# Kernel optimization log

Hardware: AMD Instinct MI355X
Metric: run time of the kernel (lower is better)

Reference implementation:

```python
import jax, jax.numpy as jnp
import numpy as np

CAPACITY_FACTOR = 1.0


def setup_inputs() -> dict:
    key = jax.random.key(0)
    k1, k2, k3 = jax.random.split(key, 3)
    x = jax.random.normal(k1, (4, 2048, 2048), jnp.float32)          # [B, S, d_model]
    wg = jax.random.normal(k2, (2048, 8), jnp.float32) * 0.02        # gate weight [d_model, E]
    we = jax.random.normal(k3, (8, 2048, 8192), jnp.float32) * 0.02  # expert weights [E, d_model, d_ff]
    be = jnp.zeros((8, 8192), jnp.float32)                           # expert bias [E, d_ff]
    return {"x": x, "wg": wg, "we": we, "be": be}


def reference(x, wg, we, be):
    d = x.shape[-1]
    tokens = x.reshape(-1, d)                       # [S, d]  (S = total tokens)
    S = tokens.shape[0]
    E = wg.shape[1]
    C = int(S * CAPACITY_FACTOR) // E               # per-expert capacity

    # ---- top-1 gate (DeepSpeed-style) -> dispatch_mask [S, E, C] ----
    logits = tokens @ wg                            # [S, E]
    gates = jax.nn.softmax(logits, axis=-1)
    idx = jnp.argmax(gates, axis=-1)                # chosen expert per token
    mask1 = jax.nn.one_hot(idx, E, dtype=tokens.dtype)        # [S, E]
    locations = jnp.cumsum(mask1, axis=0) - 1.0               # position within expert queue
    mask1 = mask1 * (locations < C).astype(tokens.dtype)      # drop tokens over capacity
    loc_s = jnp.sum(locations * mask1, axis=1).astype(jnp.int32)  # [S]
    loc_oh = jax.nn.one_hot(loc_s, C, dtype=tokens.dtype)          # [S, C]
    dispatch_mask = mask1[:, :, None] * loc_oh[:, None, :]         # [S, E, C] one-hot

    # ---- dense one-hot dispatch: einsum('sec,sm->ecm') ----
    dispatched = jnp.einsum('sec,sm->ecm', dispatch_mask, tokens)  # [E, C, d]

    # AllToAll with ep_size=1 is identity; reshape (ep_size, num_local_experts, C, d)
    dispatched = dispatched.reshape(1, E, C, d)

    # ---- front experts: per-expert Linear (front half of FFN) ----
    out = jnp.einsum('gecd,edf->gecf', dispatched, we) + be[None, :, None, :]

    return out.reshape(-1, we.shape[-1])            # [E*C, d_ff]
```

## Files before the change

kernel.cpp:

```cpp
#include <hip/hip_runtime.h>
#include <hip/hip_bf16.h>

#define S_TOK 8192
#define DM    2048
#define DFF   8192
#define NE    8
#define CAP   1024

typedef __bf16 bf16_t;
typedef __bf16 bf16x8 __attribute__((ext_vector_type(8)));
typedef float  f32x4  __attribute__((ext_vector_type(4)));

__device__ __forceinline__ void load_lds16(const void* g, void* l) {
    __builtin_amdgcn_global_load_lds((const __attribute__((address_space(1))) void*)g,
                                     (__attribute__((address_space(3))) void*)l,
                                     16, 0, 0);
}

__global__ __launch_bounds__(256) void gate_argmax(const float* __restrict__ x,
                                                   const float* __restrict__ wg,
                                                   int* __restrict__ eidx) {
    int lane = threadIdx.x & 63, wv = threadIdx.x >> 6;
    int s = blockIdx.x * 4 + wv;
    const float* row = x + (size_t)s * DM;
    float acc[8] = {0.f,0.f,0.f,0.f,0.f,0.f,0.f,0.f};
    for (int kb = 0; kb < DM; kb += 256) {
        int k0 = kb + lane * 4;
        float4 xv = *(const float4*)(row + k0);
        const float* wr = wg + (size_t)k0 * NE;
        float xs[4] = {xv.x, xv.y, xv.z, xv.w};
#pragma unroll
        for (int c = 0; c < 4; ++c) {
            float4 w0 = *(const float4*)(wr + c * 8);
            float4 w1 = *(const float4*)(wr + c * 8 + 4);
            acc[0] += xs[c] * w0.x; acc[1] += xs[c] * w0.y;
            acc[2] += xs[c] * w0.z; acc[3] += xs[c] * w0.w;
            acc[4] += xs[c] * w1.x; acc[5] += xs[c] * w1.y;
            acc[6] += xs[c] * w1.z; acc[7] += xs[c] * w1.w;
        }
    }
#pragma unroll
    for (int off = 32; off > 0; off >>= 1)
#pragma unroll
        for (int e = 0; e < 8; ++e) acc[e] += __shfl_xor(acc[e], off, 64);
    if (lane == 0) {
        float best = acc[0]; int bi = 0;
#pragma unroll
        for (int e = 1; e < 8; ++e) if (acc[e] > best) { best = acc[e]; bi = e; }
        eidx[s] = bi;
    }
}

__global__ __launch_bounds__(64) void scatter_slots(const int* __restrict__ eidx,
                                                    int* __restrict__ srcOf) {
    int lane = threadIdx.x;
    unsigned long long below = (lane == 0) ? 0ull : ((1ull << lane) - 1ull);
    for (int i = lane; i < NE * CAP; i += 64) srcOf[i] = -1;

    int cnt[NE] = {0,0,0,0,0,0,0,0};
    int e_cur = eidx[lane];
    for (int it = 0; it < S_TOK / 64; ++it) {
        int e_nxt = (it < S_TOK / 64 - 1) ? eidx[(it + 1) * 64 + lane] : 0;
        int s = it * 64 + lane;
#pragma unroll
        for (int ex = 0; ex < NE; ++ex) {
            unsigned long long m = __ballot(e_cur == ex);
            if (e_cur == ex) {
                int loc = cnt[ex] + __popcll(m & below);
                if (loc < CAP) srcOf[ex * CAP + loc] = s;
            }
            cnt[ex] += __popcll(m);
        }
        e_cur = e_nxt;
    }
}

__global__ __launch_bounds__(256) void pack_rows(const float* __restrict__ x,
                                                 const int* __restrict__ srcOf,
                                                 char* __restrict__ abuf) {
    int slot = blockIdx.x;
    int e = slot >> 10, c = slot & 1023;
    int mt = c >> 7, m = c & 127;
    int src = srcOf[slot];
    int tid = threadIdx.x;
    int kt = tid >> 3, kg = tid & 7;
    bf16x8 v = {};
    if (src >= 0) {
        const float4* p = (const float4*)(x + (size_t)src * DM + kt * 64 + kg * 8);
        float4 a = p[0], b = p[1];
        v = bf16x8{(bf16_t)a.x,(bf16_t)a.y,(bf16_t)a.z,(bf16_t)a.w,
                   (bf16_t)b.x,(bf16_t)b.y,(bf16_t)b.z,(bf16_t)b.w};
    }
    size_t img = (size_t)((e * 8 + mt) * 32 + kt) * 16384;
    int off = m * 128 + ((kg ^ (m & 7)) << 4);
    *(bf16x8*)(abuf + img + off) = v;
}

__global__ __launch_bounds__(256, 3) void moe_gemm(const char* __restrict__ abuf,
                                                   const float* __restrict__ we,
                                                   const float* __restrict__ be,
                                                   float* __restrict__ out) {
    __shared__ uint4 smem4[32768 / 16];
    char* smem = (char*)smem4;

    int bid = blockIdx.x;
    int e  = bid & 7;
    int r  = bid >> 3;
    int mt = r & 7;
    int nt = r >> 3;
    int tid = threadIdx.x, lane = tid & 63, wv = tid >> 6;
    int wm = wv >> 1, wn = wv & 1;
    int lr = lane & 15, g = lane >> 4;

    const char* aI = abuf + (size_t)((e * 8 + mt) * 32) * 16384;
    int q = tid >> 5;
    int c = (tid & 31) * 4;
    const float* bBase = we + (size_t)e * DM * DFF + (size_t)nt * 128 + c;

    f32x4 acc[4][4] = {};
    float4 bs[8];

    auto issueB = [&](int kt) {
        const float* bp = bBase + ((size_t)kt * 64 + q * 8) * DFF;
#pragma unroll
        for (int j = 0; j < 8; ++j)
            bs[j] = *(const float4*)(bp + (size_t)j * DFF);
    };
    auto writeB = [&]() {
#pragma unroll
        for (int i = 0; i < 4; ++i) {
            int n = c + i;
            bf16x8 w;
#pragma unroll
            for (int j = 0; j < 8; ++j) {
                float v = (i == 0) ? bs[j].x : (i == 1) ? bs[j].y
                        : (i == 2) ? bs[j].z : bs[j].w;
                w[j] = (bf16_t)v;
            }
            *(bf16x8*)(smem + 16384 + n * 128 + ((q ^ (n & 7)) << 4)) = w;
        }
    };
    auto stageA = [&](int kt) {
        const char* src = aI + (size_t)kt * 16384 + tid * 16;
        char* dst = smem + tid * 16;
#pragma unroll
        for (int i = 0; i < 4; ++i) load_lds16(src + i * 4096, dst + i * 4096);
    };

    issueB(0);
    stageA(0);
    writeB();
    __syncthreads();

    for (int kt = 0; kt < 32; ++kt) {
        bool nl = (kt < 31);
        if (nl) issueB(kt + 1);
        __builtin_amdgcn_sched_barrier(0);

        bf16x8 af[4][2];
#pragma unroll
        for (int mf = 0; mf < 4; ++mf) {
            int m = wm * 64 + mf * 16 + lr;
#pragma unroll
            for (int kk = 0; kk < 2; ++kk)
                af[mf][kk] = *(const bf16x8*)(smem + m * 128 + (((kk * 4 + g) ^ (m & 7)) << 4));
        }
#pragma unroll
        for (int nf = 0; nf < 4; ++nf) {
            int n = wn * 64 + nf * 16 + lr;
            bf16x8 bfr[2];
#pragma unroll
            for (int kk = 0; kk < 2; ++kk)
                bfr[kk] = *(const bf16x8*)(smem + 16384 + n * 128 + (((kk * 4 + g) ^ (n & 7)) << 4));
#pragma unroll
            for (int mf = 0; mf < 4; ++mf)
#pragma unroll
                for (int kk = 0; kk < 2; ++kk)
                    acc[mf][nf] = __builtin_amdgcn_mfma_f32_16x16x32_bf16(
                        af[mf][kk], bfr[kk], acc[mf][nf], 0, 0, 0);
        }

        if (nl) {
            __syncthreads();
            stageA(kt + 1);
            writeB();
            __syncthreads();
        }
    }

    int orow0 = e * CAP + mt * 128 + wm * 64 + g * 4;
    int ocol0 = nt * 128 + wn * 64 + lr;
#pragma unroll
    for (int nf = 0; nf < 4; ++nf) {
        int oc = ocol0 + nf * 16;
        float bias = be[(size_t)e * DFF + oc];
#pragma unroll
        for (int mf = 0; mf < 4; ++mf) {
            int orow = orow0 + mf * 16;
#pragma unroll
            for (int qq = 0; qq < 4; ++qq)
                out[(size_t)(orow + qq) * DFF + oc] = acc[mf][nf][qq] + bias;
        }
    }
}

extern "C" void kernel_launch(void* const* d_in, const int* in_sizes, int n_in,
                              void* d_out, int out_size, void* d_ws, size_t ws_size,
                              hipStream_t stream) {
    const float* x  = (const float*)d_in[0];
    const float* wg = (const float*)d_in[1];
    const float* we = (const float*)d_in[2];
    const float* be = (const float*)d_in[3];
    float* out = (float*)d_out;

    size_t need = 65536 + (size_t)32 * 1048576;
    if (ws_size < need) return;

    int* eidx  = (int*)d_ws;
    int* srcOf = eidx + S_TOK;
    char* abuf = (char*)d_ws + 65536;

    gate_argmax<<<S_TOK / 4, 256, 0, stream>>>(x, wg, eidx);
    scatter_slots<<<1, 64, 0, stream>>>(eidx, srcOf);
    pack_rows<<<S_TOK, 256, 0, stream>>>(x, srcOf, abuf);
    moe_gemm<<<NE * 8 * 64, 256, 0, stream>>>(abuf, we, be, out);
}
```

Baseline: 576.1 us.

## Widen GEMM tile to 128x256 and split B prefetch into two halves

The expert GEMM tile grows from 128x128 to 128x256, so each block stages a 256-wide B tile and each wave accumulates 4x8 MFMA fragments. This halves the grid and reuses each staged A tile across twice as many output columns. The B prefetch is split into two register batches, the second issued mid-loop after half the MFMAs, and s_setprio raises wave priority around the MFMA bursts. The cost is more registers and LDS, so occupancy drops from 3 to 2 blocks per CU, with fewer blocks in flight to hide global latency.

```diff
diff --git a/kernel.cpp b/kernel.cpp
--- a/kernel.cpp
+++ b/kernel.cpp
@@ -96,11 +96,11 @@
     *(bf16x8*)(abuf + img + off) = v;
 }
 
-__global__ __launch_bounds__(256, 3) void moe_gemm(const char* __restrict__ abuf,
+__global__ __launch_bounds__(256, 2) void moe_gemm(const char* __restrict__ abuf,
                                                    const float* __restrict__ we,
                                                    const float* __restrict__ be,
                                                    float* __restrict__ out) {
-    __shared__ uint4 smem4[32768 / 16];
+    __shared__ uint4 smem4[49152 / 16];
     char* smem = (char*)smem4;
 
     int bid = blockIdx.x;
@@ -113,28 +113,32 @@
     int lr = lane & 15, g = lane >> 4;
 
     const char* aI = abuf + (size_t)((e * 8 + mt) * 32) * 16384;
-    int q = tid >> 5;
-    int c = (tid & 31) * 4;
-    const float* bBase = we + (size_t)e * DM * DFF + (size_t)nt * 128 + c;
-
-    f32x4 acc[4][4] = {};
-    float4 bs[8];
-
-    auto issueB = [&](int kt) {
-        const float* bp = bBase + ((size_t)kt * 64 + q * 8) * DFF;
-#pragma unroll
-        for (int j = 0; j < 8; ++j)
-            bs[j] = *(const float4*)(bp + (size_t)j * DFF);
-    };
-    auto writeB = [&]() {
+    int oct = tid & 3, nq = tid >> 2;
+    const float* bBase = we + (size_t)e * DM * DFF + (size_t)nt * 256 + nq * 4;
+
+    f32x4 acc[4][8] = {};
+    float4 bs0[8], bs1[8];
+
+    auto issueB0 = [&](int kt) {
+        const float* bp = bBase + ((size_t)kt * 64 + oct * 8) * DFF;
+#pragma unroll
+        for (int j = 0; j < 8; ++j) bs0[j] = *(const float4*)(bp + (size_t)j * DFF);
+    };
+    auto issueB1 = [&](int kt) {
+        const float* bp = bBase + ((size_t)kt * 64 + 32 + oct * 8) * DFF;
+#pragma unroll
+        for (int j = 0; j < 8; ++j) bs1[j] = *(const float4*)(bp + (size_t)j * DFF);
+    };
+    auto writeB = [&](const float4* bsv, int h) {
+        int q = h * 4 + oct;
 #pragma unroll
         for (int i = 0; i < 4; ++i) {
-            int n = c + i;
+            int n = nq * 4 + i;
             bf16x8 w;
 #pragma unroll
             for (int j = 0; j < 8; ++j) {
-                float v = (i == 0) ? bs[j].x : (i == 1) ? bs[j].y
-                        : (i == 2) ? bs[j].z : bs[j].w;
+                float v = (i == 0) ? bsv[j].x : (i == 1) ? bsv[j].y
+                        : (i == 2) ? bsv[j].z : bsv[j].w;
                 w[j] = (bf16_t)v;
             }
             *(bf16x8*)(smem + 16384 + n * 128 + ((q ^ (n & 7)) << 4)) = w;
@@ -147,14 +151,16 @@
         for (int i = 0; i < 4; ++i) load_lds16(src + i * 4096, dst + i * 4096);
     };
 
-    issueB(0);
+    issueB0(0);
+    issueB1(0);
     stageA(0);
-    writeB();
+    writeB(bs0, 0);
+    writeB(bs1, 1);
     __syncthreads();
 
     for (int kt = 0; kt < 32; ++kt) {
         bool nl = (kt < 31);
-        if (nl) issueB(kt + 1);
+        if (nl) issueB0(kt + 1);
         __builtin_amdgcn_sched_barrier(0);
 
         bf16x8 af[4][2];
@@ -166,32 +172,36 @@
                 af[mf][kk] = *(const bf16x8*)(smem + m * 128 + (((kk * 4 + g) ^ (m & 7)) << 4));
         }
 #pragma unroll
-        for (int nf = 0; nf < 4; ++nf) {
-            int n = wn * 64 + nf * 16 + lr;
+        for (int nf = 0; nf < 8; ++nf) {
+            int n = wn * 128 + nf * 16 + lr;
             bf16x8 bfr[2];
 #pragma unroll
             for (int kk = 0; kk < 2; ++kk)
                 bfr[kk] = *(const bf16x8*)(smem + 16384 + n * 128 + (((kk * 4 + g) ^ (n & 7)) << 4));
+            __builtin_amdgcn_s_setprio(1);
 #pragma unroll
             for (int mf = 0; mf < 4; ++mf)
 #pragma unroll
                 for (int kk = 0; kk < 2; ++kk)
                     acc[mf][nf] = __builtin_amdgcn_mfma_f32_16x16x32_bf16(
                         af[mf][kk], bfr[kk], acc[mf][nf], 0, 0, 0);
-        }
-
+            __builtin_amdgcn_s_setprio(0);
+            if (nf == 3 && nl) issueB1(kt + 1);
+        }
+
+        __syncthreads();
         if (nl) {
-            __syncthreads();
             stageA(kt + 1);
-            writeB();
-            __syncthreads();
-        }
+            writeB(bs0, 0);
+            writeB(bs1, 1);
+        }
+        __syncthreads();
     }
 
     int orow0 = e * CAP + mt * 128 + wm * 64 + g * 4;
-    int ocol0 = nt * 128 + wn * 64 + lr;
-#pragma unroll
-    for (int nf = 0; nf < 4; ++nf) {
+    int ocol0 = nt * 256 + wn * 128 + lr;
+#pragma unroll
+    for (int nf = 0; nf < 8; ++nf) {
         int oc = ocol0 + nf * 16;
         float bias = be[(size_t)e * DFF + oc];
 #pragma unroll
@@ -223,5 +233,5 @@
     gate_argmax<<<S_TOK / 4, 256, 0, stream>>>(x, wg, eidx);
     scatter_slots<<<1, 64, 0, stream>>>(eidx, srcOf);
     pack_rows<<<S_TOK, 256, 0, stream>>>(x, srcOf, abuf);
-    moe_gemm<<<NE * 8 * 64, 256, 0, stream>>>(abuf, we, be, out);
-}
+    moe_gemm<<<NE * 8 * 32, 256, 0, stream>>>(abuf, we, be, out);
+}
```

Result: slower. 743.8 us (+29.1%).
